# Kernel optimization log

Hardware: AMD Instinct MI355X
Metric: run time of the kernel (lower is better)

Reference implementation:

```python
import jax, jax.numpy as jnp
import numpy as np

K = 5
PAD = K // 2
MARGIN = 0.3
EPS_AFF = 1e-9


def setup_inputs() -> dict:
    key = jax.random.key(0)
    k1, k2 = jax.random.split(key)
    pred = jax.random.normal(k1, (4, 64, 192, 640), dtype=jnp.float32)
    target = jax.random.randint(k2, (4, 1, 192, 640), 0, 20, dtype=jnp.int32)
    return {"pred": pred, "target": target}


def _loss_map(pred, target):
    # pred: [B,C,h,w] float, target: [B,1,h,w] int labels (same spatial size
    # as pred, so the nearest-neighbor interpolate in torch is the identity).
    B, C, h, w = pred.shape
    center = target  # [B,1,h,w]
    # label padding uses value=-1 (never matches a real label)
    pad_lbl = jnp.pad(center, ((0, 0), (0, 0), (PAD, PAD), (PAD, PAD)),
                      constant_values=-1)
    # F.normalize(feature, dim=1): x / max(||x||, 1e-12)
    norm = jnp.sqrt(jnp.sum(pred * pred, axis=1, keepdims=True))
    feat = pred / jnp.maximum(norm, 1e-12)
    pad_feat = jnp.pad(feat, ((0, 0), (0, 0), (PAD, PAD), (PAD, PAD)))

    labels, sims = [], []
    for i in range(K):          # fixed 5x5 window, 25 shifted slices
        for j in range(K):
            sh_lbl = pad_lbl[:, :, i:i + h, j:j + w]
            labels.append(center == sh_lbl)
            sh_feat = pad_feat[:, :, i:i + h, j:j + w]
            sims.append(jnp.sum(feat * sh_feat, axis=1, keepdims=True))
    agg = jnp.stack(labels, axis=-1).astype(jnp.float32)  # [B,1,h,w,25]
    sim = jnp.stack(sims, axis=-1)                          # [B,1,h,w,25]

    pos = agg
    neg = 1.0 - agg
    pos_num = jnp.sum(pos, axis=-1)   # [B,1,h,w]; >= 1 (center matches itself)
    neg_num = jnp.sum(neg, axis=-1)
    boundary = (pos_num >= K - 1) & (neg_num >= K - 1)

    affinity = jnp.sqrt(jnp.maximum(EPS_AFF, 2.0 - 2.0 * sim))  # [B,1,h,w,25]
    pos_dist = jnp.sum(pos * affinity, axis=-1) / pos_num
    neg_dist = jnp.sum(neg * affinity, axis=-1) / jnp.maximum(neg_num, 1e-12)

    triplet = jnp.maximum(0.0, pos_dist - neg_dist + MARGIN)
    # torch does boolean indexing loss_map = max(0, ...)[boundary]; we keep the
    # static-shape equivalent: full map zeroed outside the boundary region.
    return jnp.where(boundary, triplet, 0.0)


def reference(pred, target):
    return _loss_map(pred, target)
```

## Files before the change

kernel.cpp:

```cpp
#include <hip/hip_runtime.h>

constexpr int Bn = 4, Cn = 64, Hn = 192, Wn = 640, HW = Hn * Wn;
constexpr int TH = 8, TW = 64;
constexpr int SH = TH + 4;
constexpr int SW = TW + 4;
constexpr int NS = SH * SW;
constexpr int NP = NS / 2;
constexpr int PPR = SW / 2;
constexpr int NT = 512;
constexpr int CH = 4;
constexpr int NCHUNK = Cn / CH;
constexpr int DR = SH - 2;
constexpr int ND = DR * SW;
constexpr int NPAIR = (DR / 2) * SW;
constexpr int ARENA = 12 * ND;

__global__ __launch_bounds__(NT, 4) void guide_triplet_kernel(
    const float* __restrict__ pred,
    const int*   __restrict__ target,
    float* __restrict__ out)
{
    __shared__ float arena[ARENA];
    __shared__ float invnS[NS + 4];
    __shared__ int   lblS[NS];

    const int x0 = blockIdx.x * TW;
    const int y0 = blockIdx.y * TH;
    const int b  = blockIdx.z;

    const int tid = threadIdx.x;
    const int tx  = tid & (TW - 1);
    const int ty  = tid >> 6;

    const bool hasS = (tid < NP);
    const int srow = tid / PPR;
    const int spc  = tid - srow * PPR;
    const int gy = y0 + srow - 2;
    const int gx = x0 + 2 * spc - 2;
    const bool okS = hasS && (gy >= 0) && (gy < Hn) && (gx >= 0) && (gx + 1 < Wn);
    const int goff = gy * Wn + gx;
    const int sidx = 2 * tid;

    if (hasS) {
        int lx = -1, ly = -1;
        if (okS) {
            const int2 L = *reinterpret_cast<const int2*>(target + b * HW + goff);
            lx = L.x; ly = L.y;
        }
        lblS[sidx]     = lx;
        lblS[sidx + 1] = ly;
    }
    if (tid < 4) invnS[NS + tid] = 1.0f;

    const bool isPair = (tid < NPAIR);
    const int pa = tid / SW;
    const int pc = tid - pa * SW;
    const int rA = 2 * pa;

    float ssx = 0.0f, ssy = 0.0f;
    float accA[12], accB[12];
    #pragma unroll
    for (int i = 0; i < 12; ++i) { accA[i] = 0.0f; accB[i] = 0.0f; }

    const float* predb = pred + (size_t)b * Cn * HW;

    float2 ldA[CH], ldB[CH];

#define LOADCHUNK(DST, CHUNK) do {                                          \
    _Pragma("unroll")                                                       \
    for (int cc = 0; cc < CH; ++cc) {                                       \
        const float* pc_ = predb + (size_t)((CHUNK) * CH + cc) * HW;        \
        float2 v = make_float2(0.f, 0.f);                                   \
        if (okS) v = *reinterpret_cast<const float2*>(pc_ + goff);          \
        DST[cc] = v;                                                        \
    } } while (0)

#define BODY(K, LD, KP2) {                                                  \
    float* sb = arena + ((K) & 1) * (CH * NS);                              \
                          \
    if (hasS) {                                                             \
        _Pragma("unroll")                                                   \
        for (int cc = 0; cc < CH; ++cc) {                                   \
            const float2 v = LD[cc];                                        \
            *reinterpret_cast<float2*>(&sb[cc * NS + sidx]) = v;            \
            ssx = fmaf(v.x, v.x, ssx);                                      \
            ssy = fmaf(v.y, v.y, ssy);                                      \
        } }                                                                 \
    __syncthreads();                                                        \
                         \
    if ((KP2) < NCHUNK) LOADCHUNK(LD, KP2);                                 \
        \
    if (isPair) {                                                           \
        _Pragma("unroll")                                                   \
        for (int cc = 0; cc < CH; ++cc) {                                   \
            const float* s0 = sb + cc * NS + rA * SW + pc;                  \
            const float w00 = s0[0], w01 = s0[1], w02 = s0[2];              \
            const float* s1 = s0 + (SW - 2);                                \
            const float w10 = s1[0], w11 = s1[1], w12 = s1[2],              \
                        w13 = s1[3], w14 = s1[4];                           \
            const float* s2 = s1 + SW;                                      \
            const float w20 = s2[0], w21 = s2[1], w22 = s2[2],              \
                        w23 = s2[3], w24 = s2[4];                           \
            const float* s3 = s2 + SW;                                      \
            const float w30 = s3[0], w31 = s3[1], w32 = s3[2],              \
                        w33 = s3[3], w34 = s3[4];                           \
            accA[0]  = fmaf(w00, w01, accA[0]);                             \
            accA[1]  = fmaf(w00, w02, accA[1]);                             \
            accA[2]  = fmaf(w00, w10, accA[2]);                             \
            accA[3]  = fmaf(w00, w11, accA[3]);                             \
            accA[4]  = fmaf(w00, w12, accA[4]);                             \
            accA[5]  = fmaf(w00, w13, accA[5]);                             \
            accA[6]  = fmaf(w00, w14, accA[6]);                             \
            accA[7]  = fmaf(w00, w20, accA[7]);                             \
            accA[8]  = fmaf(w00, w21, accA[8]);                             \
            accA[9]  = fmaf(w00, w22, accA[9]);                             \
            accA[10] = fmaf(w00, w23, accA[10]);                            \
            accA[11] = fmaf(w00, w24, accA[11]);                            \
            accB[0]  = fmaf(w12, w13, accB[0]);                             \
            accB[1]  = fmaf(w12, w14, accB[1]);                             \
            accB[2]  = fmaf(w12, w20, accB[2]);                             \
            accB[3]  = fmaf(w12, w21, accB[3]);                             \
            accB[4]  = fmaf(w12, w22, accB[4]);                             \
            accB[5]  = fmaf(w12, w23, accB[5]);                             \
            accB[6]  = fmaf(w12, w24, accB[6]);                             \
            accB[7]  = fmaf(w12, w30, accB[7]);                             \
            accB[8]  = fmaf(w12, w31, accB[8]);                             \
            accB[9]  = fmaf(w12, w32, accB[9]);                             \
            accB[10] = fmaf(w12, w33, accB[10]);                            \
            accB[11] = fmaf(w12, w34, accB[11]);                            \
        } } }

    LOADCHUNK(ldA, 0);
    LOADCHUNK(ldB, 1);

    for (int chunk = 0; chunk < NCHUNK; chunk += 2) {
        BODY(chunk,     ldA, chunk + 2)
        BODY(chunk + 1, ldB, chunk + 3)
    }

    if (hasS) {
        invnS[sidx]     = 1.0f / fmaxf(sqrtf(ssx), 1e-12f);
        invnS[sidx + 1] = 1.0f / fmaxf(sqrtf(ssy), 1e-12f);
    }
    __syncthreads();

    constexpr int DIRD[12] = {1, 2, SW - 2, SW - 1, SW, SW + 1, SW + 2,
                              2 * SW - 2, 2 * SW - 1, 2 * SW, 2 * SW + 1, 2 * SW + 2};

    if (isPair) {
        const int qA = rA * SW + pc;
        const int qB = qA + SW;
        const float icA = invnS[qA];
        const float icB = invnS[qB];
        #pragma unroll
        for (int k = 0; k < 12; ++k) {
            const int dq = DIRD[k];
            const float simA = accA[k] * icA * invnS[qA + dq];
            const float simB = accB[k] * icB * invnS[qB + dq];
            arena[k * ND + qA] = sqrtf(fmaxf(1e-9f, fmaf(-2.0f, simA, 2.0f)));
            arena[k * ND + qB] = sqrtf(fmaxf(1e-9f, fmaf(-2.0f, simB, 2.0f)));
        }
    }
    __syncthreads();

    const int qp = (2 + ty) * SW + (2 + tx);
    const int lc = lblS[qp];

    float tot = 0.0f, ps = 0.0f, pn = 0.0f;
    #pragma unroll
    for (int k = 0; k < 12; ++k) {
        const int dq = DIRD[k];
        const float affF = arena[k * ND + qp];
        const float affB = arena[k * ND + qp - dq];
        const float mfF = (lblS[qp + dq] == lc) ? 1.0f : 0.0f;
        const float mfB = (lblS[qp - dq] == lc) ? 1.0f : 0.0f;
        tot += affF + affB;
        pn += mfF + mfB;
        ps = fmaf(mfF, affF, fmaf(mfB, affB, ps));
    }
    const float pos_num = pn + 1.0f;
    const float pos_sum = ps + 3.16227766e-5f;
    const float neg_num = 24.0f - pn;
    const float neg_sum = tot - ps;
    const bool boundary = (pos_num >= 4.0f) && (neg_num >= 4.0f);
    const float tri = fmaxf(0.0f,
        pos_sum / pos_num - neg_sum / fmaxf(neg_num, 1e-12f) + 0.3f);
    out[((size_t)b * Hn + (y0 + ty)) * Wn + (x0 + tx)] = boundary ? tri : 0.0f;
}

extern "C" void kernel_launch(void* const* d_in, const int* in_sizes, int n_in,
                              void* d_out, int out_size, void* d_ws, size_t ws_size,
                              hipStream_t stream) {
    const float* pred   = (const float*)d_in[0];
    const int*   target = (const int*)d_in[1];
    float*       out    = (float*)d_out;
    dim3 grid(Wn / TW, Hn / TH, Bn);
    guide_triplet_kernel<<<grid, NT, 0, stream>>>(pred, target, out);
}
```

Baseline: 67.66 us.

## Move halo staging to upper threads with 4-wide loads, single-chunk prefetch

Staging of pred and labels into shared memory now uses the last NQ threads, with each thread handling four consecutive pixels through two float2 global loads and one float4 LDS store. Before, the first NS/2 threads handled two pixels each. Because the pair-compute threads are the low tids, the loading work now falls on mostly different waves from the FMA work, which may improve overlap and reduce per-wave imbalance. Prefetch depth drops from two chunks ahead to one, which lowers register pressure but reduces latency hiding.

```diff
diff --git a/kernel.cpp b/kernel.cpp
--- a/kernel.cpp
+++ b/kernel.cpp
@@ -2,17 +2,17 @@
 
 constexpr int Bn = 4, Cn = 64, Hn = 192, Wn = 640, HW = Hn * Wn;
 constexpr int TH = 8, TW = 64;
-constexpr int SH = TH + 4;
-constexpr int SW = TW + 4;
+constexpr int SH = TH + 4, SW = TW + 4;
 constexpr int NS = SH * SW;
-constexpr int NP = NS / 2;
-constexpr int PPR = SW / 2;
 constexpr int NT = 512;
 constexpr int CH = 4;
 constexpr int NCHUNK = Cn / CH;
 constexpr int DR = SH - 2;
 constexpr int ND = DR * SW;
 constexpr int NPAIR = (DR / 2) * SW;
+constexpr int NQ = NS / 4;
+constexpr int QPR = SW / 4;
+constexpr int SBASE = NT - NQ;
 constexpr int ARENA = 12 * ND;
 
 __global__ __launch_bounds__(NT, 4) void guide_triplet_kernel(
@@ -20,9 +20,9 @@
     const int*   __restrict__ target,
     float* __restrict__ out)
 {
-    __shared__ float arena[ARENA];
-    __shared__ float invnS[NS + 4];
-    __shared__ int   lblS[NS];
+    __shared__ alignas(16) float arena[ARENA];
+    __shared__ alignas(16) float invnS[NS + 4];
+    __shared__ alignas(16) int   lblS[NS];
 
     const int x0 = blockIdx.x * TW;
     const int y0 = blockIdx.y * TH;
@@ -32,23 +32,24 @@
     const int tx  = tid & (TW - 1);
     const int ty  = tid >> 6;
 
-    const bool hasS = (tid < NP);
-    const int srow = tid / PPR;
-    const int spc  = tid - srow * PPR;
-    const int gy = y0 + srow - 2;
-    const int gx = x0 + 2 * spc - 2;
-    const bool okS = hasS && (gy >= 0) && (gy < Hn) && (gx >= 0) && (gx + 1 < Wn);
+    const bool hasS = (tid >= SBASE);
+    const int j    = tid - SBASE;
+    const int qrow = j / QPR;
+    const int qcol = 4 * (j - qrow * QPR);
+    const int gy = y0 + qrow - 2;
+    const int gx = x0 + qcol - 2;
+    const bool gyok = (gy >= 0) && (gy < Hn);
+    const bool ok0 = hasS && gyok && (gx >= 0) && (gx + 1 < Wn);
+    const bool ok1 = hasS && gyok && (gx + 2 >= 0) && (gx + 3 < Wn);
     const int goff = gy * Wn + gx;
-    const int sidx = 2 * tid;
+    const int sidx = 4 * j;
 
     if (hasS) {
-        int lx = -1, ly = -1;
-        if (okS) {
-            const int2 L = *reinterpret_cast<const int2*>(target + b * HW + goff);
-            lx = L.x; ly = L.y;
-        }
-        lblS[sidx]     = lx;
-        lblS[sidx + 1] = ly;
+        const int* tb = target + b * HW;
+        int4 L = make_int4(-1, -1, -1, -1);
+        if (ok0) { const int2 t = *reinterpret_cast<const int2*>(tb + goff);     L.x = t.x; L.y = t.y; }
+        if (ok1) { const int2 t = *reinterpret_cast<const int2*>(tb + goff + 2); L.z = t.x; L.w = t.y; }
+        *reinterpret_cast<int4*>(&lblS[sidx]) = L;
     }
     if (tid < 4) invnS[NS + tid] = 1.0f;
 
@@ -57,39 +58,43 @@
     const int pc = tid - pa * SW;
     const int rA = 2 * pa;
 
-    float ssx = 0.0f, ssy = 0.0f;
+    float ss[4] = {0.f, 0.f, 0.f, 0.f};
     float accA[12], accB[12];
     #pragma unroll
     for (int i = 0; i < 12; ++i) { accA[i] = 0.0f; accB[i] = 0.0f; }
 
     const float* predb = pred + (size_t)b * Cn * HW;
 
-    float2 ldA[CH], ldB[CH];
-
-#define LOADCHUNK(DST, CHUNK) do {                                          \
+    float2 ld[CH][2];
+
+#define LOADCHUNK(CHUNK) do {                                               \
     _Pragma("unroll")                                                       \
     for (int cc = 0; cc < CH; ++cc) {                                       \
         const float* pc_ = predb + (size_t)((CHUNK) * CH + cc) * HW;        \
-        float2 v = make_float2(0.f, 0.f);                                   \
-        if (okS) v = *reinterpret_cast<const float2*>(pc_ + goff);          \
-        DST[cc] = v;                                                        \
+        float2 v0 = make_float2(0.f, 0.f), v1 = make_float2(0.f, 0.f);      \
+        if (ok0) v0 = *reinterpret_cast<const float2*>(pc_ + goff);         \
+        if (ok1) v1 = *reinterpret_cast<const float2*>(pc_ + goff + 2);     \
+        ld[cc][0] = v0; ld[cc][1] = v1;                                     \
     } } while (0)
 
-#define BODY(K, LD, KP2) {                                                  \
+#define BODY(K) {                                                           \
     float* sb = arena + ((K) & 1) * (CH * NS);                              \
-                          \
+               \
     if (hasS) {                                                             \
         _Pragma("unroll")                                                   \
         for (int cc = 0; cc < CH; ++cc) {                                   \
-            const float2 v = LD[cc];                                        \
-            *reinterpret_cast<float2*>(&sb[cc * NS + sidx]) = v;            \
-            ssx = fmaf(v.x, v.x, ssx);                                      \
-            ssy = fmaf(v.y, v.y, ssy);                                      \
+            const float4 w = make_float4(ld[cc][0].x, ld[cc][0].y,          \
+                                         ld[cc][1].x, ld[cc][1].y);         \
+            *reinterpret_cast<float4*>(&sb[cc * NS + sidx]) = w;            \
+            ss[0] = fmaf(w.x, w.x, ss[0]);                                  \
+            ss[1] = fmaf(w.y, w.y, ss[1]);                                  \
+            ss[2] = fmaf(w.z, w.z, ss[2]);                                  \
+            ss[3] = fmaf(w.w, w.w, ss[3]);                                  \
         } }                                                                 \
     __syncthreads();                                                        \
-                         \
-    if ((KP2) < NCHUNK) LOADCHUNK(LD, KP2);                                 \
-        \
+    \
+    if ((K) + 1 < NCHUNK) LOADCHUNK((K) + 1);                               \
+       \
     if (isPair) {                                                           \
         _Pragma("unroll")                                                   \
         for (int cc = 0; cc < CH; ++cc) {                                   \
@@ -130,17 +135,20 @@
             accB[11] = fmaf(w12, w34, accB[11]);                            \
         } } }
 
-    LOADCHUNK(ldA, 0);
-    LOADCHUNK(ldB, 1);
+    LOADCHUNK(0);
 
     for (int chunk = 0; chunk < NCHUNK; chunk += 2) {
-        BODY(chunk,     ldA, chunk + 2)
-        BODY(chunk + 1, ldB, chunk + 3)
+        BODY(chunk)
+        BODY(chunk + 1)
     }
 
     if (hasS) {
-        invnS[sidx]     = 1.0f / fmaxf(sqrtf(ssx), 1e-12f);
-        invnS[sidx + 1] = 1.0f / fmaxf(sqrtf(ssy), 1e-12f);
+        float4 iv;
+        iv.x = 1.0f / fmaxf(sqrtf(ss[0]), 1e-12f);
+        iv.y = 1.0f / fmaxf(sqrtf(ss[1]), 1e-12f);
+        iv.z = 1.0f / fmaxf(sqrtf(ss[2]), 1e-12f);
+        iv.w = 1.0f / fmaxf(sqrtf(ss[3]), 1e-12f);
+        *reinterpret_cast<float4*>(&invnS[sidx]) = iv;
     }
     __syncthreads();
 
```

New measurement: 67.73 us. No clear change (+0.1%).
